# Kernel tuning notes

Hardware: AMD Instinct MI355X
Metric: run time of the kernel (lower is better)

## Reference

```python
import jax, jax.numpy as jnp
import numpy as np

B, IN, FS, S, H = 4096, 4096, 4096, 64, 512  # batch, input_size, first_size, shape_lstm, n_hidden
D = FS // S  # per-step feature for left/right (=64); up/down per-step feature = S (=64)


def _lstm_cell(x, h, c, Wih, Whh, bih, bhh):
    # standard torch LSTMCell gate order: i, f, g, o
    g = x @ Wih.T + bih + h @ Whh.T + bhh  # (B, 4H)
    i, f, gg, o = jnp.split(g, 4, axis=-1)
    c = jax.nn.sigmoid(f) * c + jax.nn.sigmoid(i) * jnp.tanh(gg)
    h = jax.nn.sigmoid(o) * jnp.tanh(c)
    return h, c


def setup_inputs() -> dict:
    key = jax.random.key(0)
    ks = jax.random.split(key, 20)
    def cell(k, d_in):
        k1, k2, k3, k4 = jax.random.split(k, 4)
        s = 1.0 / np.sqrt(H)
        return (jax.random.uniform(k1, (4 * H, d_in), jnp.float32, -s, s),
                jax.random.uniform(k2, (4 * H, H), jnp.float32, -s, s),
                jax.random.uniform(k3, (4 * H,), jnp.float32, -s, s),
                jax.random.uniform(k4, (4 * H,), jnp.float32, -s, s))
    Wih_l, Whh_l, bih_l, bhh_l = cell(ks[0], D)
    Wih_r, Whh_r, bih_r, bhh_r = cell(ks[1], D)
    Wih_d, Whh_d, bih_d, bhh_d = cell(ks[2], S)
    return {
        "x": jax.random.normal(ks[3], (B, IN), jnp.float32),
        "h0": jax.random.normal(ks[4], (4, B, H), jnp.float32),
        "c0": jax.random.normal(ks[5], (4, B, H), jnp.float32),
        "W1": jax.random.normal(ks[6], (FS, IN), jnp.float32) * (1.0 / np.sqrt(IN)),
        "b1": jnp.zeros((FS,), jnp.float32),
        "Wih_l": Wih_l, "Whh_l": Whh_l, "bih_l": bih_l, "bhh_l": bhh_l,
        "Wih_r": Wih_r, "Whh_r": Whh_r, "bih_r": bih_r, "bhh_r": bhh_r,
        "Wih_d": Wih_d, "Whh_d": Whh_d, "bih_d": bih_d, "bhh_d": bhh_d,
        "W3": jax.random.normal(ks[7], (10, 4 * H), jnp.float32) * (1.0 / np.sqrt(4 * H)),
        "b3": jnp.zeros((10,), jnp.float32),
    }


def reference(x, h0, c0, W1, b1, Wih_l, Whh_l, bih_l, bhh_l,
              Wih_r, Whh_r, bih_r, bhh_r, Wih_d, Whh_d, bih_d, bhh_d, W3, b3):
    feat = jax.nn.relu(x @ W1.T + b1)            # (B, FS); dropout=identity (eval)
    il = feat.reshape(B, S, D)
    x_left = jnp.transpose(il, (1, 0, 2))         # (S, B, D)
    x_right = x_left[::-1]
    x_up = jnp.transpose(il, (2, 0, 1))           # (D, B, S); loop uses first S steps
    x_down = x_up[::-1]

    def step(carry, xs):
        (hl, cl, hr, cr, hu, cu, hd, cd) = carry
        xl, xr, xu, xd = xs
        hl, cl = _lstm_cell(xl, hl, cl, Wih_l, Whh_l, bih_l, bhh_l)
        hr, cr = _lstm_cell(xr, hr, cr, Wih_r, Whh_r, bih_r, bhh_r)
        # original code uses the DOWN cell for both up and down directions
        hu, cu = _lstm_cell(xu, hu, cu, Wih_d, Whh_d, bih_d, bhh_d)
        hd, cd = _lstm_cell(xd, hd, cd, Wih_d, Whh_d, bih_d, bhh_d)
        return (hl, cl, hr, cr, hu, cu, hd, cd), None

    carry0 = (h0[0], c0[0], h0[1], c0[1], h0[2], c0[2], h0[3], c0[3])
    (hl, _, hr, _, hu, _, hd, _), _ = jax.lax.scan(
        step, carry0, (x_left[:S], x_right[:S], x_up[:S], x_down[:S]))
    out = jnp.concatenate([hl, hr, hu, hd], axis=1)  # (B, 4H)
    logits = out @ W3.T + b3
    return jax.nn.log_softmax(logits, axis=1)
```

## Files before the change

### kernel.cpp

```cpp
#include <hip/hip_runtime.h>
#include <cstddef>
#include <cstdint>

namespace {

constexpr int kB  = 4096;
constexpr int kIN = 4096;
constexpr int kFS = 4096;
constexpr int kS  = 64;
constexpr int kH  = 512;
constexpr int kNG = 2048;
constexpr int kKC = 576;

typedef __bf16 bf16_t;
typedef __bf16 bfrag  __attribute__((ext_vector_type(8)));
typedef __bf16 bf16v4 __attribute__((ext_vector_type(4)));
typedef float  f32x4  __attribute__((ext_vector_type(4)));

__device__ __forceinline__ void gload16(const void* g, void* l) {
  __builtin_amdgcn_global_load_lds(
      (const __attribute__((address_space(1))) void*)g,
      (__attribute__((address_space(3))) void*)l, 16, 0, 0);
}

__device__ __forceinline__ float sigf(float x) { return 1.0f / (1.0f + __expf(-x)); }
__device__ __forceinline__ float tanh_fast(float x) {
  float e = __expf(2.0f * x);
  return 1.0f - 2.0f / (e + 1.0f);
}

__device__ __forceinline__ f32x4 mfma16(bfrag a, bfrag b, f32x4 c) {
  return __builtin_amdgcn_mfma_f32_16x16x32_bf16(a, b, c, 0, 0, 0);
}


__global__ __launch_bounds__(256) void f2b4_kernel(const float* __restrict__ in,
                                                   bf16_t* __restrict__ out, int n4) {
  int i = blockIdx.x * 256 + threadIdx.x;
  if (i >= n4) return;
  float4 v = reinterpret_cast<const float4*>(in)[i];
  bf16v4 o = {(bf16_t)v.x, (bf16_t)v.y, (bf16_t)v.z, (bf16_t)v.w};
  *reinterpret_cast<bf16v4*>(out + (size_t)i * 4) = o;
}

__global__ __launch_bounds__(256) void pack_wcat2_kernel(
    const float* __restrict__ Wih_l, const float* __restrict__ Whh_l,
    const float* __restrict__ Wih_r, const float* __restrict__ Whh_r,
    const float* __restrict__ Wih_d, const float* __restrict__ Whh_d,
    bf16_t* __restrict__ wcat2) {
  const int total = 3 * 128 * 9 * 2 * 64 * 8;
  int idx = blockIdx.x * 256 + threadIdx.x;
  if (idx >= total) return;
  int e  = idx & 7;
  int l  = (idx >> 3) & 63;
  int kk = (idx >> 9) & 1;
  int r  = idx >> 10;
  int kt = r % 9;
  int matnb = r / 9;
  int mat = matnb >> 7;
  int nb  = matnb & 127;
  const int c = nb * 16 + (l & 15);
  const int g = (c >> 4) & 3;
  const int u = (c >> 6) * 16 + (c & 15);
  const int orow = g * kH + u;
  const int k = kt * 64 + kk * 32 + (l >> 4) * 8 + e;
  const float* Wih = (mat == 0) ? Wih_l : (mat == 1) ? Wih_r : Wih_d;
  const float* Whh = (mat == 0) ? Whh_l : (mat == 1) ? Whh_r : Whh_d;
  float v = (k < 64) ? Wih[(size_t)orow * 64 + k] : Whh[(size_t)orow * 512 + (k - 64)];
  wcat2[idx] = (bf16_t)v;
}

__global__ __launch_bounds__(256) void pack_bias_kernel(
    const float* __restrict__ bih_l, const float* __restrict__ bhh_l,
    const float* __restrict__ bih_r, const float* __restrict__ bhh_r,
    const float* __restrict__ bih_d, const float* __restrict__ bhh_d,
    float* __restrict__ biasc) {
  int idx = blockIdx.x * 256 + threadIdx.x;
  if (idx >= 3 * kNG) return;
  int mat = idx / kNG;
  int c = idx - mat * kNG;
  int g = (c >> 4) & 3;
  int u = (c >> 6) * 16 + (c & 15);
  int orow = g * kH + u;
  const float* bi = (mat == 0) ? bih_l : (mat == 1) ? bih_r : bih_d;
  const float* bh = (mat == 0) ? bhh_l : (mat == 1) ? bhh_r : bhh_d;
  biasc[idx] = bi[orow] + bh[orow];
}

__global__ __launch_bounds__(256) void pack_hc_kernel(const float* __restrict__ h0,
                                                      const float* __restrict__ c0,
                                                      bf16_t* __restrict__ hbuf0,
                                                      float* __restrict__ cbuf, int n) {
  int i = blockIdx.x * 256 + threadIdx.x;
  if (i >= n) return;
  hbuf0[i] = (bf16_t)h0[i];
  cbuf[i]  = c0[i];
}

__global__ __launch_bounds__(256) void transpose64_kernel(const bf16_t* __restrict__ feat,
                                                          bf16_t* __restrict__ featT) {
  __shared__ bf16_t tile[64][65];
  const int b = blockIdx.x;
  const bf16_t* src = feat + (size_t)b * kFS;
  bf16_t* dst = featT + (size_t)b * kFS;
  for (int i = threadIdx.x; i < 4096; i += 256) tile[i >> 6][i & 63] = src[i];
  __syncthreads();
  for (int i = threadIdx.x; i < 4096; i += 256) dst[i] = tile[i & 63][i >> 6];
}


__global__ __launch_bounds__(256, 4) void gemm_feat_kernel(
    const bf16_t* __restrict__ X, const bf16_t* __restrict__ W,
    const float* __restrict__ b1, bf16_t* __restrict__ feat) {
  __shared__ bf16_t As[128 * 32];
  __shared__ bf16_t Bs[128 * 32];
  const int t = threadIdx.x;
  const int bid = blockIdx.x;
  const int widx = (bid & 7) * 128 + (bid >> 3);
  const int bm = widx & 31, bn = widx >> 5;
  const int w = t >> 6, l = t & 63;
  const int wm = (w >> 1) * 64, wn = (w & 1) * 64;
  const int sr = t >> 2;
  const int skS = ((t & 3) ^ ((t >> 3) & 3)) * 8;
  const int lr = l & 15;
  const int lkS = ((l >> 4) ^ ((l >> 1) & 3)) * 8;
  const int lrow4 = (l >> 4) * 4;

  f32x4 acc[4][4];
#pragma unroll
  for (int i = 0; i < 4; ++i)
#pragma unroll
    for (int j = 0; j < 4; ++j) acc[i][j] = (f32x4){0.f, 0.f, 0.f, 0.f};

  const bf16_t* ga = X + (size_t)(bm * 128 + sr) * kIN + skS;
  const bf16_t* gb = W + (size_t)(bn * 128 + sr) * kIN + skS;
  bf16_t* lA = As + w * 512;
  bf16_t* lB = Bs + w * 512;

  for (int kt = 0; kt < kIN / 32; ++kt) {
    gload16(ga, lA);
    gload16(ga + (size_t)64 * kIN, lA + 2048);
    gload16(gb, lB);
    gload16(gb + (size_t)64 * kIN, lB + 2048);
    ga += 32; gb += 32;
    __syncthreads();
    bfrag a[4], b[4];
#pragma unroll
    for (int mi = 0; mi < 4; ++mi)
      a[mi] = *reinterpret_cast<const bfrag*>(&As[(wm + mi * 16 + lr) * 32 + lkS]);
#pragma unroll
    for (int ni = 0; ni < 4; ++ni)
      b[ni] = *reinterpret_cast<const bfrag*>(&Bs[(wn + ni * 16 + lr) * 32 + lkS]);
#pragma unroll
    for (int mi = 0; mi < 4; ++mi)
#pragma unroll
      for (int ni = 0; ni < 4; ++ni)
        acc[mi][ni] = __builtin_amdgcn_mfma_f32_16x16x32_bf16(a[mi], b[ni], acc[mi][ni], 0, 0, 0);
    __syncthreads();
  }

#pragma unroll
  for (int ni = 0; ni < 4; ++ni) {
    const int col = bn * 128 + wn + ni * 16 + lr;
    const float bb = b1[col];
#pragma unroll
    for (int mi = 0; mi < 4; ++mi) {
#pragma unroll
      for (int r = 0; r < 4; ++r) {
        const int row = bm * 128 + wm + mi * 16 + lrow4 + r;
        float v = acc[mi][ni][r] + bb;
        feat[(size_t)row * kFS + col] = (bf16_t)fmaxf(v, 0.0f);
      }
    }
  }
}


__global__ __launch_bounds__(512, 1) void lstm_step_kernel(
    const bf16_t* __restrict__ feat, const bf16_t* __restrict__ featT,
    const bf16_t* __restrict__ wcat2, const float* __restrict__ biasc,
    const bf16_t* __restrict__ hin, bf16_t* __restrict__ hout,
    float* __restrict__ cbuf, int s) {
  extern __shared__ __align__(16) char smem[];

  const int t = threadIdx.x;
  const int l = t & 63, w = t >> 6;
  const int wr = w >> 2, wc = w & 3;
  const int lr = l & 15, lq = l >> 4;
  const int sx = lr & 7;
  const int srow = l >> 3;
  const int sslot = (l & 7) ^ (srow & 7);

  const int bid = blockIdx.x;
  const int widx = (bid & 7) * 64 + (bid >> 3);
  const int cell = widx >> 7;
  const int rwk = widx & 127;
  const int bm = rwk >> 3, bn = rwk & 7;

  const bf16_t* xsrc = (cell < 2) ? feat : featT;
  const int off = ((cell & 1) ? (63 - s) : s) * 64;
  const int mat = (cell < 2) ? cell : 2;
  const bf16_t* hc = hin + (size_t)cell * kB * kH;

  auto stageA = [&](int kt, int buf) {
    bf16_t* base = (bf16_t*)(smem + buf * 32768);
#pragma unroll
    for (int j = 0; j < 4; ++j) {
      const int row0 = j * 64 + w * 8;
      bf16_t* dst = base + row0 * 64;
      const bf16_t* src = (kt == 0)
          ? xsrc + (size_t)(bm * 256 + row0 + srow) * kFS + off + sslot * 8
          : hc + (size_t)(bm * 256 + row0 + srow) * kH + (kt - 1) * 64 + sslot * 8;
      gload16(src, dst);
    }
  };

  const size_t wb0 = ((size_t)mat * 128 + bn * 16 + wc * 4) * 9;
  auto loadB = [&](int kt, bfrag (&d)[8]) {
#pragma unroll
    for (int nn = 0; nn < 4; ++nn)
#pragma unroll
      for (int kk = 0; kk < 2; ++kk)
        d[nn * 2 + kk] = *reinterpret_cast<const bfrag*>(
            wcat2 + (((wb0 + (size_t)nn * 9 + kt) * 2 + kk) << 9) + l * 8);
  };

  f32x4 acc[8][4];
#pragma unroll
  for (int i = 0; i < 8; ++i)
#pragma unroll
    for (int j = 0; j < 4; ++j) acc[i][j] = (f32x4){0.f, 0.f, 0.f, 0.f};

  bfrag bA[8], bB[8];

  stageA(0, 0);
  loadB(0, bA);
  asm volatile("s_waitcnt vmcnt(0)" ::: "memory");
  __builtin_amdgcn_sched_barrier(0);
  __builtin_amdgcn_s_barrier();

#pragma unroll
  for (int kt = 0; kt < 9; ++kt) {
    const int cur = kt & 1;
    const bf16_t* As_ = (const bf16_t*)(smem + cur * 32768);
    bfrag (&bCur)[8] = (kt & 1) ? bB : bA;
    bfrag (&bNxt)[8] = (kt & 1) ? bA : bB;

    if (kt < 8) stageA(kt + 1, cur ^ 1);

    bfrag a[8];
#pragma unroll
    for (int mi = 0; mi < 4; ++mi)
#pragma unroll
      for (int kk = 0; kk < 2; ++kk)
        a[mi * 2 + kk] = *reinterpret_cast<const bfrag*>(
            As_ + (wr * 128 + mi * 16 + lr) * 64 + (((kk * 4 + lq) ^ sx) * 8));
    __builtin_amdgcn_s_setprio(1);
#pragma unroll
    for (int kk = 0; kk < 2; ++kk)
#pragma unroll
      for (int mi = 0; mi < 4; ++mi)
#pragma unroll
        for (int nn = 0; nn < 4; ++nn)
          acc[mi][nn] = mfma16(a[mi * 2 + kk], bCur[nn * 2 + kk], acc[mi][nn]);
    __builtin_amdgcn_s_setprio(0);

    if (kt < 8) loadB(kt + 1, bNxt);

#pragma unroll
    for (int mi = 0; mi < 4; ++mi)
#pragma unroll
      for (int kk = 0; kk < 2; ++kk)
        a[mi * 2 + kk] = *reinterpret_cast<const bfrag*>(
            As_ + (wr * 128 + 64 + mi * 16 + lr) * 64 + (((kk * 4 + lq) ^ sx) * 8));
    __builtin_amdgcn_s_setprio(1);
#pragma unroll
    for (int kk = 0; kk < 2; ++kk)
#pragma unroll
      for (int mi = 0; mi < 4; ++mi)
#pragma unroll
        for (int nn = 0; nn < 4; ++nn)
          acc[4 + mi][nn] = mfma16(a[mi * 2 + kk], bCur[nn * 2 + kk], acc[4 + mi][nn]);
    __builtin_amdgcn_s_setprio(0);
    __builtin_amdgcn_sched_barrier(0);

    if (kt < 8) {
      asm volatile("s_waitcnt vmcnt(8)" ::: "memory");
      __builtin_amdgcn_sched_barrier(0);
      __builtin_amdgcn_s_barrier();
    }
  }

  const float* biasn = biasc + mat * kNG + bn * 256 + wc * 64;
  const float bb0 = biasn[0 * 16 + lr];
  const float bb1 = biasn[1 * 16 + lr];
  const float bb2 = biasn[2 * 16 + lr];
  const float bb3 = biasn[3 * 16 + lr];
  const int u = (bn * 4 + wc) * 16 + lr;
  const int row0 = bm * 256 + wr * 128 + lq * 4;
#pragma unroll
  for (int mi = 0; mi < 8; ++mi) {
#pragma unroll
    for (int j = 0; j < 4; ++j) {
      const float iv = sigf(acc[mi][0][j] + bb0);
      const float fv = sigf(acc[mi][1][j] + bb1);
      const float gv = tanh_fast(acc[mi][2][j] + bb2);
      const float ov = sigf(acc[mi][3][j] + bb3);
      const int row = row0 + mi * 16 + j;
      const size_t cidx = ((size_t)cell * kB + row) * kH + u;
      const float cn = fv * cbuf[cidx] + iv * gv;
      cbuf[cidx] = cn;
      hout[cidx] = (bf16_t)(ov * tanh_fast(cn));
    }
  }
}


__global__ __launch_bounds__(256) void head_kernel(const bf16_t* __restrict__ hfin,
                                                   const float* __restrict__ W3,
                                                   const float* __restrict__ b3,
                                                   float* __restrict__ out) {
  const int b = blockIdx.x, t = threadIdx.x;
  const int l = t & 63, w = t >> 6;
  float acc[10];
#pragma unroll
  for (int j = 0; j < 10; ++j) acc[j] = 0.f;
  for (int k = t; k < 2048; k += 256) {
    const int cell = k >> 9, u = k & 511;
    const float hv = (float)hfin[((size_t)cell * kB + b) * kH + u];
#pragma unroll
    for (int j = 0; j < 10; ++j) acc[j] += hv * W3[j * 2048 + k];
  }
#pragma unroll
  for (int j = 0; j < 10; ++j)
#pragma unroll
    for (int o = 32; o > 0; o >>= 1) acc[j] += __shfl_down(acc[j], o, 64);
  __shared__ float wred[4][10];
  if (l == 0)
#pragma unroll
    for (int j = 0; j < 10; ++j) wred[w][j] = acc[j];
  __syncthreads();
  if (t == 0) {
    float logits[10];
#pragma unroll
    for (int j = 0; j < 10; ++j)
      logits[j] = wred[0][j] + wred[1][j] + wred[2][j] + wred[3][j] + b3[j];
    float mx = logits[0];
#pragma unroll
    for (int j = 1; j < 10; ++j) mx = fmaxf(mx, logits[j]);
    float se = 0.f;
#pragma unroll
    for (int j = 0; j < 10; ++j) se += expf(logits[j] - mx);
    const float lse = mx + logf(se);
#pragma unroll
    for (int j = 0; j < 10; ++j) out[(size_t)b * 10 + j] = logits[j] - lse;
  }
}

}

extern "C" void kernel_launch(void* const* d_in, const int* in_sizes, int n_in,
                              void* d_out, int out_size, void* d_ws, size_t ws_size,
                              hipStream_t stream) {
  const float* x     = (const float*)d_in[0];
  const float* h0    = (const float*)d_in[1];
  const float* c0    = (const float*)d_in[2];
  const float* W1    = (const float*)d_in[3];
  const float* b1    = (const float*)d_in[4];
  const float* Wih_l = (const float*)d_in[5];
  const float* Whh_l = (const float*)d_in[6];
  const float* bih_l = (const float*)d_in[7];
  const float* bhh_l = (const float*)d_in[8];
  const float* Wih_r = (const float*)d_in[9];
  const float* Whh_r = (const float*)d_in[10];
  const float* bih_r = (const float*)d_in[11];
  const float* bhh_r = (const float*)d_in[12];
  const float* Wih_d = (const float*)d_in[13];
  const float* Whh_d = (const float*)d_in[14];
  const float* bih_d = (const float*)d_in[15];
  const float* bhh_d = (const float*)d_in[16];
  const float* W3    = (const float*)d_in[17];
  const float* b3    = (const float*)d_in[18];
  float* out = (float*)d_out;

  char* p = (char*)d_ws;
  auto take = [&](size_t bytes) {
    char* r = p;
    p += (bytes + 255) & ~(size_t)255;
    return r;
  };
  bf16_t* xb    = (bf16_t*)take((size_t)kB * kIN * 2);
  bf16_t* w1b   = (bf16_t*)take((size_t)kFS * kIN * 2);
  bf16_t* feat  = (bf16_t*)take((size_t)kB * kFS * 2);
  bf16_t* wcat2 = (bf16_t*)take((size_t)3 * 128 * 9 * 2 * 64 * 8 * 2);
  float*  biasc = (float*)take((size_t)3 * kNG * 4);
  float*  cbuf  = (float*)take((size_t)4 * kB * kH * 4);
  bf16_t* featT = xb;
  bf16_t* hbuf  = w1b;
  const size_t HSZ = (size_t)4 * kB * kH;

  (void)hipFuncSetAttribute(reinterpret_cast<const void*>(&lstm_step_kernel),
                            hipFuncAttributeMaxDynamicSharedMemorySize, 65536);

  f2b4_kernel<<<(kB * kIN / 4) / 256, 256, 0, stream>>>(x, xb, kB * kIN / 4);
  f2b4_kernel<<<(kFS * kIN / 4) / 256, 256, 0, stream>>>(W1, w1b, kFS * kIN / 4);
  gemm_feat_kernel<<<dim3(1024), 256, 0, stream>>>(xb, w1b, b1, feat);
  transpose64_kernel<<<kB, 256, 0, stream>>>(feat, featT);
  {
    const int total = 3 * 128 * 9 * 2 * 64 * 8;
    pack_wcat2_kernel<<<(total + 255) / 256, 256, 0, stream>>>(
        Wih_l, Whh_l, Wih_r, Whh_r, Wih_d, Whh_d, wcat2);
  }
  pack_bias_kernel<<<(3 * kNG + 255) / 256, 256, 0, stream>>>(
      bih_l, bhh_l, bih_r, bhh_r, bih_d, bhh_d, biasc);
  pack_hc_kernel<<<(int)(HSZ / 256), 256, 0, stream>>>(h0, c0, hbuf, cbuf, (int)HSZ);

  for (int s = 0; s < 64; ++s) {
    lstm_step_kernel<<<dim3(512), 512, 65536, stream>>>(
        feat, featT, wcat2, biasc,
        hbuf + (size_t)(s & 1) * HSZ, hbuf + (size_t)((s + 1) & 1) * HSZ, cbuf, s);
  }
  head_kernel<<<kB, 256, 0, stream>>>(hbuf, W3, b3, out);
}
```

Measured before the change: 3.834 ms.

## Fuse all 64 LSTM steps into one persistent kernel with h kept in LDS

Replaces the 64 per-step LSTM launches with a single persistent kernel of 256 blocks. Each block owns 64 batch rows of one direction across all gate columns, so the recurrent hidden state stays in shared memory and no global h round-trip or inter-block sync is needed. h0/c0 packing is folded into the kernel, and the cell state is kept in a block-private layout in global memory. In exchange, only 256 blocks run, and all weights are streamed from global/L2 every step by each block, which may lower parallelism and raise weight traffic.

```diff
diff --git a/kernel.cpp b/kernel.cpp
--- a/kernel.cpp
+++ b/kernel.cpp
@@ -11,6 +11,7 @@
 constexpr int kH  = 512;
 constexpr int kNG = 2048;
 constexpr int kKC = 576;
+constexpr int kRowB = 1152;
 
 typedef __bf16 bf16_t;
 typedef __bf16 bfrag  __attribute__((ext_vector_type(8)));
@@ -28,9 +29,12 @@
   float e = __expf(2.0f * x);
   return 1.0f - 2.0f / (e + 1.0f);
 }
-
 __device__ __forceinline__ f32x4 mfma16(bfrag a, bfrag b, f32x4 c) {
   return __builtin_amdgcn_mfma_f32_16x16x32_bf16(a, b, c, 0, 0, 0);
+}
+__device__ __forceinline__ unsigned short bf16bits(float v) {
+  __bf16 b = (__bf16)v;
+  return __builtin_bit_cast(unsigned short, b);
 }
 
 
@@ -87,16 +91,6 @@
   biasc[idx] = bi[orow] + bh[orow];
 }
 
-__global__ __launch_bounds__(256) void pack_hc_kernel(const float* __restrict__ h0,
-                                                      const float* __restrict__ c0,
-                                                      bf16_t* __restrict__ hbuf0,
-                                                      float* __restrict__ cbuf, int n) {
-  int i = blockIdx.x * 256 + threadIdx.x;
-  if (i >= n) return;
-  hbuf0[i] = (bf16_t)h0[i];
-  cbuf[i]  = c0[i];
-}
-
 __global__ __launch_bounds__(256) void transpose64_kernel(const bf16_t* __restrict__ feat,
                                                           bf16_t* __restrict__ featT) {
   __shared__ bf16_t tile[64][65];
@@ -176,142 +170,166 @@
 }
 
 
-__global__ __launch_bounds__(512, 1) void lstm_step_kernel(
+__global__ __launch_bounds__(512, 1) void lstm_all_kernel(
     const bf16_t* __restrict__ feat, const bf16_t* __restrict__ featT,
     const bf16_t* __restrict__ wcat2, const float* __restrict__ biasc,
-    const bf16_t* __restrict__ hin, bf16_t* __restrict__ hout,
-    float* __restrict__ cbuf, int s) {
+    const float* __restrict__ h0, const float* __restrict__ c0,
+    float* __restrict__ cbuf, bf16_t* __restrict__ hfin) {
   extern __shared__ __align__(16) char smem[];
 
   const int t = threadIdx.x;
   const int l = t & 63, w = t >> 6;
-  const int wr = w >> 2, wc = w & 3;
   const int lr = l & 15, lq = l >> 4;
   const int sx = lr & 7;
-  const int srow = l >> 3;
-  const int sslot = (l & 7) ^ (srow & 7);
+  const int e0 = lq ^ sx;
+  const int e1 = (4 + lq) ^ sx;
 
   const int bid = blockIdx.x;
-  const int widx = (bid & 7) * 64 + (bid >> 3);
-  const int cell = widx >> 7;
-  const int rwk = widx & 127;
-  const int bm = rwk >> 3, bn = rwk & 7;
-
+  const int cell = (bid & 7) >> 1;
+  const int rb = ((bid & 7) & 1) * 32 + (bid >> 3);
+  const int row0 = rb * 64;
+  const int mat = (cell < 2) ? cell : 2;
   const bf16_t* xsrc = (cell < 2) ? feat : featT;
-  const int off = ((cell & 1) ? (63 - s) : s) * 64;
-  const int mat = (cell < 2) ? cell : 2;
-  const bf16_t* hc = hin + (size_t)cell * kB * kH;
-
-  auto stageA = [&](int kt, int buf) {
-    bf16_t* base = (bf16_t*)(smem + buf * 32768);
-#pragma unroll
-    for (int j = 0; j < 4; ++j) {
-      const int row0 = j * 64 + w * 8;
-      bf16_t* dst = base + row0 * 64;
-      const bf16_t* src = (kt == 0)
-          ? xsrc + (size_t)(bm * 256 + row0 + srow) * kFS + off + sslot * 8
-          : hc + (size_t)(bm * 256 + row0 + srow) * kH + (kt - 1) * 64 + sslot * 8;
-      gload16(src, dst);
-    }
-  };
-
-  const size_t wb0 = ((size_t)mat * 128 + bn * 16 + wc * 4) * 9;
-  auto loadB = [&](int kt, bfrag (&d)[8]) {
+
+  const char* aBase[4][2];
+#pragma unroll
+  for (int mi = 0; mi < 4; ++mi) {
+    const int rowb = (mi * 16 + lr) * kRowB;
+    aBase[mi][0] = smem + rowb + e0 * 16;
+    aBase[mi][1] = smem + rowb + e1 * 16;
+  }
+
+  const size_t nbBase = (size_t)mat * 128 + w * 4;
+  auto loadB = [&](int ch, int kt, bfrag (&d)[8]) {
 #pragma unroll
     for (int nn = 0; nn < 4; ++nn)
 #pragma unroll
       for (int kk = 0; kk < 2; ++kk)
         d[nn * 2 + kk] = *reinterpret_cast<const bfrag*>(
-            wcat2 + (((wb0 + (size_t)nn * 9 + kt) * 2 + kk) << 9) + l * 8);
+            wcat2 + ((((nbBase + ch * 32 + nn) * 9 + kt) * 2 + kk) << 9) + l * 8);
   };
 
-  f32x4 acc[8][4];
-#pragma unroll
-  for (int i = 0; i < 8; ++i)
+  {
+    const int xr = t >> 3, xs_ = t & 7;
+    bfrag xv = *reinterpret_cast<const bfrag*>(
+        xsrc + (size_t)(row0 + xr) * kFS + ((cell & 1) ? 63 : 0) * 64 + xs_ * 8);
+    *reinterpret_cast<bfrag*>(smem + xr * kRowB + ((xs_ ^ (xr & 7)) * 16)) = xv;
+    const int u0 = (t & 7) * 64;
+    const float* hp = h0 + ((size_t)cell * kB + row0 + xr) * kH + u0;
+#pragma unroll
+    for (int i = 0; i < 8; ++i) {
+      bfrag hv;
+#pragma unroll
+      for (int e = 0; e < 8; ++e) hv[e] = (bf16_t)hp[i * 8 + e];
+      const int sl = (8 + (u0 >> 3) + i) ^ (xr & 7);
+      *reinterpret_cast<bfrag*>(smem + xr * kRowB + sl * 16) = hv;
+    }
+  }
+  __syncthreads();
+
+  f32x4 acc[4][4];
+#pragma unroll
+  for (int i = 0; i < 4; ++i)
 #pragma unroll
     for (int j = 0; j < 4; ++j) acc[i][j] = (f32x4){0.f, 0.f, 0.f, 0.f};
 
-  bfrag bA[8], bB[8];
-
-  stageA(0, 0);
-  loadB(0, bA);
-  asm volatile("s_waitcnt vmcnt(0)" ::: "memory");
-  __builtin_amdgcn_sched_barrier(0);
-  __builtin_amdgcn_s_barrier();
-
-#pragma unroll
-  for (int kt = 0; kt < 9; ++kt) {
-    const int cur = kt & 1;
-    const bf16_t* As_ = (const bf16_t*)(smem + cur * 32768);
-    bfrag (&bCur)[8] = (kt & 1) ? bB : bA;
-    bfrag (&bNxt)[8] = (kt & 1) ? bA : bB;
-
-    if (kt < 8) stageA(kt + 1, cur ^ 1);
-
-    bfrag a[8];
-#pragma unroll
-    for (int mi = 0; mi < 4; ++mi)
-#pragma unroll
-      for (int kk = 0; kk < 2; ++kk)
-        a[mi * 2 + kk] = *reinterpret_cast<const bfrag*>(
-            As_ + (wr * 128 + mi * 16 + lr) * 64 + (((kk * 4 + lq) ^ sx) * 8));
-    __builtin_amdgcn_s_setprio(1);
-#pragma unroll
-    for (int kk = 0; kk < 2; ++kk)
-#pragma unroll
-      for (int mi = 0; mi < 4; ++mi)
-#pragma unroll
-        for (int nn = 0; nn < 4; ++nn)
-          acc[mi][nn] = mfma16(a[mi * 2 + kk], bCur[nn * 2 + kk], acc[mi][nn]);
-    __builtin_amdgcn_s_setprio(0);
-
-    if (kt < 8) loadB(kt + 1, bNxt);
-
-#pragma unroll
-    for (int mi = 0; mi < 4; ++mi)
-#pragma unroll
-      for (int kk = 0; kk < 2; ++kk)
-        a[mi * 2 + kk] = *reinterpret_cast<const bfrag*>(
-            As_ + (wr * 128 + 64 + mi * 16 + lr) * 64 + (((kk * 4 + lq) ^ sx) * 8));
-    __builtin_amdgcn_s_setprio(1);
-#pragma unroll
-    for (int kk = 0; kk < 2; ++kk)
-#pragma unroll
-      for (int mi = 0; mi < 4; ++mi)
-#pragma unroll
-        for (int nn = 0; nn < 4; ++nn)
-          acc[4 + mi][nn] = mfma16(a[mi * 2 + kk], bCur[nn * 2 + kk], acc[4 + mi][nn]);
-    __builtin_amdgcn_s_setprio(0);
-    __builtin_amdgcn_sched_barrier(0);
-
-    if (kt < 8) {
-      asm volatile("s_waitcnt vmcnt(8)" ::: "memory");
-      __builtin_amdgcn_sched_barrier(0);
-      __builtin_amdgcn_s_barrier();
+  bfrag bE[8], bO[8];
+  unsigned hpk[4][8];
+  loadB(0, 0, bE);
+
+#pragma unroll 1
+  for (int s = 0; s < 64; ++s) {
+#pragma unroll
+    for (int ch = 0; ch < 4; ++ch) {
+#pragma unroll
+      for (int kt = 0; kt < 9; ++kt) {
+        const int i = ch * 9 + kt;
+        bfrag (&bc)[8] = (i & 1) ? bO : bE;
+        bfrag (&bn_)[8] = (i & 1) ? bE : bO;
+        if (i < 35) loadB((i + 1) / 9, (i + 1) % 9, bn_);
+        else        loadB(0, 0, bn_);
+        bfrag a[8];
+#pragma unroll
+        for (int mi = 0; mi < 4; ++mi) {
+          a[mi * 2 + 0] = *reinterpret_cast<const bfrag*>(aBase[mi][0] + kt * 128);
+          a[mi * 2 + 1] = *reinterpret_cast<const bfrag*>(aBase[mi][1] + kt * 128);
+        }
+#pragma unroll
+        for (int kk = 0; kk < 2; ++kk)
+#pragma unroll
+          for (int mi = 0; mi < 4; ++mi)
+#pragma unroll
+            for (int nn = 0; nn < 4; ++nn)
+              acc[mi][nn] = mfma16(a[mi * 2 + kk], bc[nn * 2 + kk], acc[mi][nn]);
+      }
+      {
+        const float* bbp = biasc + mat * kNG + ch * 512 + w * 64;
+        const float bb0 = bbp[lr], bb1 = bbp[16 + lr], bb2 = bbp[32 + lr], bb3 = bbp[48 + lr];
+        const int u = (ch * 8 + w) * 16 + lr;
+        float* cp = cbuf + ((((size_t)bid * 4 + ch) * 8 + w) * 64 + l) * 16;
+#pragma unroll
+        for (int mi = 0; mi < 4; ++mi) {
+          float cv[4];
+          if (s == 0) {
+            const float* c0p = c0 + ((size_t)cell * kB + row0 + mi * 16 + lq * 4) * kH + u;
+#pragma unroll
+            for (int j = 0; j < 4; ++j) cv[j] = c0p[(size_t)j * kH];
+          } else {
+            float4 c4 = reinterpret_cast<const float4*>(cp)[mi];
+            cv[0] = c4.x; cv[1] = c4.y; cv[2] = c4.z; cv[3] = c4.w;
+          }
+          float hv[4];
+#pragma unroll
+          for (int j = 0; j < 4; ++j) {
+            const float iv = sigf(acc[mi][0][j] + bb0);
+            const float fv = sigf(acc[mi][1][j] + bb1);
+            const float gv = tanh_fast(acc[mi][2][j] + bb2);
+            const float ov = sigf(acc[mi][3][j] + bb3);
+            const float cn = fv * cv[j] + iv * gv;
+            cv[j] = cn;
+            hv[j] = ov * tanh_fast(cn);
+          }
+          reinterpret_cast<float4*>(cp)[mi] = make_float4(cv[0], cv[1], cv[2], cv[3]);
+          if (s < 63) {
+            hpk[ch][mi * 2 + 0] = (unsigned)bf16bits(hv[0]) | ((unsigned)bf16bits(hv[1]) << 16);
+            hpk[ch][mi * 2 + 1] = (unsigned)bf16bits(hv[2]) | ((unsigned)bf16bits(hv[3]) << 16);
+          } else {
+#pragma unroll
+            for (int j = 0; j < 4; ++j)
+              hfin[((size_t)cell * kB + row0 + mi * 16 + lq * 4 + j) * kH + u] = (bf16_t)hv[j];
+          }
+#pragma unroll
+          for (int nn = 0; nn < 4; ++nn) acc[mi][nn] = (f32x4){0.f, 0.f, 0.f, 0.f};
+        }
+      }
     }
-  }
-
-  const float* biasn = biasc + mat * kNG + bn * 256 + wc * 64;
-  const float bb0 = biasn[0 * 16 + lr];
-  const float bb1 = biasn[1 * 16 + lr];
-  const float bb2 = biasn[2 * 16 + lr];
-  const float bb3 = biasn[3 * 16 + lr];
-  const int u = (bn * 4 + wc) * 16 + lr;
-  const int row0 = bm * 256 + wr * 128 + lq * 4;
-#pragma unroll
-  for (int mi = 0; mi < 8; ++mi) {
-#pragma unroll
-    for (int j = 0; j < 4; ++j) {
-      const float iv = sigf(acc[mi][0][j] + bb0);
-      const float fv = sigf(acc[mi][1][j] + bb1);
-      const float gv = tanh_fast(acc[mi][2][j] + bb2);
-      const float ov = sigf(acc[mi][3][j] + bb3);
-      const int row = row0 + mi * 16 + j;
-      const size_t cidx = ((size_t)cell * kB + row) * kH + u;
-      const float cn = fv * cbuf[cidx] + iv * gv;
-      cbuf[cidx] = cn;
-      hout[cidx] = (bf16_t)(ov * tanh_fast(cn));
+    __syncthreads();
+    if (s < 63) {
+#pragma unroll
+      for (int ch = 0; ch < 4; ++ch) {
+        const int u = (ch * 8 + w) * 16 + lr;
+        const int sl = 8 + (u >> 3);
+        const int eb = (u & 7) * 2;
+#pragma unroll
+        for (int mi = 0; mi < 4; ++mi)
+#pragma unroll
+          for (int p = 0; p < 2; ++p) {
+            const unsigned v = hpk[ch][mi * 2 + p];
+            const int r0 = mi * 16 + lq * 4 + p * 2;
+            *reinterpret_cast<uint16_t*>(smem + r0 * kRowB + ((sl ^ (r0 & 7)) * 16) + eb) =
+                (uint16_t)v;
+            const int r1 = r0 + 1;
+            *reinterpret_cast<uint16_t*>(smem + r1 * kRowB + ((sl ^ (r1 & 7)) * 16) + eb) =
+                (uint16_t)(v >> 16);
+          }
+      }
+      const int xr = t >> 3, xs_ = t & 7;
+      const int offn = ((cell & 1) ? (63 - (s + 1)) : (s + 1)) * 64;
+      bfrag xv = *reinterpret_cast<const bfrag*>(
+          xsrc + (size_t)(row0 + xr) * kFS + offn + xs_ * 8);
+      *reinterpret_cast<bfrag*>(smem + xr * kRowB + ((xs_ ^ (xr & 7)) * 16)) = xv;
     }
+    __syncthreads();
   }
 }
 
@@ -396,11 +414,10 @@
   float*  biasc = (float*)take((size_t)3 * kNG * 4);
   float*  cbuf  = (float*)take((size_t)4 * kB * kH * 4);
   bf16_t* featT = xb;
-  bf16_t* hbuf  = w1b;
-  const size_t HSZ = (size_t)4 * kB * kH;
-
-  (void)hipFuncSetAttribute(reinterpret_cast<const void*>(&lstm_step_kernel),
-                            hipFuncAttributeMaxDynamicSharedMemorySize, 65536);
+  bf16_t* hfin  = w1b;
+
+  (void)hipFuncSetAttribute(reinterpret_cast<const void*>(&lstm_all_kernel),
+                            hipFuncAttributeMaxDynamicSharedMemorySize, 64 * kRowB);
 
   f2b4_kernel<<<(kB * kIN / 4) / 256, 256, 0, stream>>>(x, xb, kB * kIN / 4);
   f2b4_kernel<<<(kFS * kIN / 4) / 256, 256, 0, stream>>>(W1, w1b, kFS * kIN / 4);
@@ -413,12 +430,9 @@
   }
   pack_bias_kernel<<<(3 * kNG + 255) / 256, 256, 0, stream>>>(
       bih_l, bhh_l, bih_r, bhh_r, bih_d, bhh_d, biasc);
-  pack_hc_kernel<<<(int)(HSZ / 256), 256, 0, stream>>>(h0, c0, hbuf, cbuf, (int)HSZ);
-
-  for (int s = 0; s < 64; ++s) {
-    lstm_step_kernel<<<dim3(512), 512, 65536, stream>>>(
-        feat, featT, wcat2, biasc,
-        hbuf + (size_t)(s & 1) * HSZ, hbuf + (size_t)((s + 1) & 1) * HSZ, cbuf, s);
-  }
-  head_kernel<<<kB, 256, 0, stream>>>(hbuf, W3, b3, out);
-}
+
+  lstm_all_kernel<<<dim3(256), 512, 64 * kRowB, stream>>>(
+      feat, featT, wcat2, biasc, h0, c0, cbuf, hfin);
+
+  head_kernel<<<kB, 256, 0, stream>>>(hfin, W3, b3, out);
+}
```

Result: slower. 13.80 ms (+259.8%).

## Shrink LSTM step tiles to 128x128 with 256-thread blocks for occupancy

Applied to the files above, without the earlier changes.

Each LSTM step block now covers a 128-row by 128-gate-column tile using 4 waves, replacing the 256x256 tile and 8 waves, so the grid grows from 512 to 2048 blocks and targets 3 blocks per CU with half the LDS. The next B-fragment prefetch is also issued before the MFMA work rather than midway through it. The aim is more resident waves to hide global-load latency and better balance across CUs. The trade-off is less reuse of A and B per block, so more redundant global and L2 traffic for weights and activations.

```diff
diff --git a/kernel.cpp b/kernel.cpp
--- a/kernel.cpp
+++ b/kernel.cpp
@@ -28,7 +28,6 @@
   float e = __expf(2.0f * x);
   return 1.0f - 2.0f / (e + 1.0f);
 }
-
 __device__ __forceinline__ f32x4 mfma16(bfrag a, bfrag b, f32x4 c) {
   return __builtin_amdgcn_mfma_f32_16x16x32_bf16(a, b, c, 0, 0, 0);
 }
@@ -176,7 +175,7 @@
 }
 
 
-__global__ __launch_bounds__(512, 1) void lstm_step_kernel(
+__global__ __launch_bounds__(256, 3) void lstm_step_kernel(
     const bf16_t* __restrict__ feat, const bf16_t* __restrict__ featT,
     const bf16_t* __restrict__ wcat2, const float* __restrict__ biasc,
     const bf16_t* __restrict__ hin, bf16_t* __restrict__ hout,
@@ -185,17 +184,17 @@
 
   const int t = threadIdx.x;
   const int l = t & 63, w = t >> 6;
-  const int wr = w >> 2, wc = w & 3;
+  const int wr = w >> 1, wcn = w & 1;
   const int lr = l & 15, lq = l >> 4;
   const int sx = lr & 7;
   const int srow = l >> 3;
-  const int sslot = (l & 7) ^ (srow & 7);
+  const int sslot = (l & 7) ^ srow;
 
   const int bid = blockIdx.x;
-  const int widx = (bid & 7) * 64 + (bid >> 3);
-  const int cell = widx >> 7;
-  const int rwk = widx & 127;
-  const int bm = rwk >> 3, bn = rwk & 7;
+  const int widx = (bid & 7) * 256 + (bid >> 3);
+  const int cell = widx >> 9;
+  const int rwk = widx & 511;
+  const int bm = rwk >> 4, bn = rwk & 15;
 
   const bf16_t* xsrc = (cell < 2) ? feat : featT;
   const int off = ((cell & 1) ? (63 - s) : s) * 64;
@@ -203,38 +202,38 @@
   const bf16_t* hc = hin + (size_t)cell * kB * kH;
 
   auto stageA = [&](int kt, int buf) {
-    bf16_t* base = (bf16_t*)(smem + buf * 32768);
+    bf16_t* base = (bf16_t*)(smem + buf * 16384);
 #pragma unroll
     for (int j = 0; j < 4; ++j) {
-      const int row0 = j * 64 + w * 8;
+      const int row0 = j * 32 + w * 8;
       bf16_t* dst = base + row0 * 64;
       const bf16_t* src = (kt == 0)
-          ? xsrc + (size_t)(bm * 256 + row0 + srow) * kFS + off + sslot * 8
-          : hc + (size_t)(bm * 256 + row0 + srow) * kH + (kt - 1) * 64 + sslot * 8;
+          ? xsrc + (size_t)(bm * 128 + row0 + srow) * kFS + off + sslot * 8
+          : hc + (size_t)(bm * 128 + row0 + srow) * kH + (kt - 1) * 64 + sslot * 8;
       gload16(src, dst);
     }
   };
 
-  const size_t wb0 = ((size_t)mat * 128 + bn * 16 + wc * 4) * 9;
+  const size_t nbB = (size_t)mat * 128 + bn * 8 + wcn * 4;
   auto loadB = [&](int kt, bfrag (&d)[8]) {
 #pragma unroll
     for (int nn = 0; nn < 4; ++nn)
 #pragma unroll
       for (int kk = 0; kk < 2; ++kk)
         d[nn * 2 + kk] = *reinterpret_cast<const bfrag*>(
-            wcat2 + (((wb0 + (size_t)nn * 9 + kt) * 2 + kk) << 9) + l * 8);
+            wcat2 + ((((nbB + nn) * 9 + kt) * 2 + kk) << 9) + l * 8);
   };
 
-  f32x4 acc[8][4];
-#pragma unroll
-  for (int i = 0; i < 8; ++i)
+  f32x4 acc[4][4];
+#pragma unroll
+  for (int i = 0; i < 4; ++i)
 #pragma unroll
     for (int j = 0; j < 4; ++j) acc[i][j] = (f32x4){0.f, 0.f, 0.f, 0.f};
 
-  bfrag bA[8], bB[8];
+  bfrag bE[8], bO[8];
 
   stageA(0, 0);
-  loadB(0, bA);
+  loadB(0, bE);
   asm volatile("s_waitcnt vmcnt(0)" ::: "memory");
   __builtin_amdgcn_sched_barrier(0);
   __builtin_amdgcn_s_barrier();
@@ -242,48 +241,30 @@
 #pragma unroll
   for (int kt = 0; kt < 9; ++kt) {
     const int cur = kt & 1;
-    const bf16_t* As_ = (const bf16_t*)(smem + cur * 32768);
-    bfrag (&bCur)[8] = (kt & 1) ? bB : bA;
-    bfrag (&bNxt)[8] = (kt & 1) ? bA : bB;
-
-    if (kt < 8) stageA(kt + 1, cur ^ 1);
-
-    bfrag a[8];
-#pragma unroll
-    for (int mi = 0; mi < 4; ++mi)
-#pragma unroll
-      for (int kk = 0; kk < 2; ++kk)
-        a[mi * 2 + kk] = *reinterpret_cast<const bfrag*>(
-            As_ + (wr * 128 + mi * 16 + lr) * 64 + (((kk * 4 + lq) ^ sx) * 8));
-    __builtin_amdgcn_s_setprio(1);
-#pragma unroll
-    for (int kk = 0; kk < 2; ++kk)
+    if (kt < 8) {
+      stageA(kt + 1, cur ^ 1);
+      __builtin_amdgcn_sched_barrier(0);
+      if (kt & 1) loadB(kt + 1, bE); else loadB(kt + 1, bO);
+      __builtin_amdgcn_sched_barrier(0);
+    }
+    const bf16_t* As_ = (const bf16_t*)(smem + cur * 16384);
+#pragma unroll
+    for (int kk = 0; kk < 2; ++kk) {
+      bfrag a[4];
 #pragma unroll
       for (int mi = 0; mi < 4; ++mi)
+        a[mi] = *reinterpret_cast<const bfrag*>(
+            As_ + (wr * 64 + mi * 16 + lr) * 64 + (((kk * 4 + lq) ^ sx) * 8));
+      __builtin_amdgcn_s_setprio(1);
+#pragma unroll
+      for (int mi = 0; mi < 4; ++mi)
 #pragma unroll
         for (int nn = 0; nn < 4; ++nn)
-          acc[mi][nn] = mfma16(a[mi * 2 + kk], bCur[nn * 2 + kk], acc[mi][nn]);
-    __builtin_amdgcn_s_setprio(0);
-
-    if (kt < 8) loadB(kt + 1, bNxt);
-
-#pragma unroll
-    for (int mi = 0; mi < 4; ++mi)
-#pragma unroll
-      for (int kk = 0; kk < 2; ++kk)
-        a[mi * 2 + kk] = *reinterpret_cast<const bfrag*>(
-            As_ + (wr * 128 + 64 + mi * 16 + lr) * 64 + (((kk * 4 + lq) ^ sx) * 8));
-    __builtin_amdgcn_s_setprio(1);
-#pragma unroll
-    for (int kk = 0; kk < 2; ++kk)
-#pragma unroll
-      for (int mi = 0; mi < 4; ++mi)
-#pragma unroll
-        for (int nn = 0; nn < 4; ++nn)
-          acc[4 + mi][nn] = mfma16(a[mi * 2 + kk], bCur[nn * 2 + kk], acc[4 + mi][nn]);
-    __builtin_amdgcn_s_setprio(0);
+          acc[mi][nn] = (kt & 1) ? mfma16(a[mi], bO[nn * 2 + kk], acc[mi][nn])
+                                 : mfma16(a[mi], bE[nn * 2 + kk], acc[mi][nn]);
+      __builtin_amdgcn_s_setprio(0);
+    }
     __builtin_amdgcn_sched_barrier(0);
-
     if (kt < 8) {
       asm volatile("s_waitcnt vmcnt(8)" ::: "memory");
       __builtin_amdgcn_sched_barrier(0);
@@ -291,22 +272,23 @@
     }
   }
 
-  const float* biasn = biasc + mat * kNG + bn * 256 + wc * 64;
-  const float bb0 = biasn[0 * 16 + lr];
-  const float bb1 = biasn[1 * 16 + lr];
-  const float bb2 = biasn[2 * 16 + lr];
-  const float bb3 = biasn[3 * 16 + lr];
-  const int u = (bn * 4 + wc) * 16 + lr;
-  const int row0 = bm * 256 + wr * 128 + lq * 4;
-#pragma unroll
-  for (int mi = 0; mi < 8; ++mi) {
+  const int nb0 = bn * 8 + wcn * 4;
+  const float* bbp = biasc + mat * kNG + nb0 * 16;
+  const float bb0 = bbp[lr];
+  const float bb1 = bbp[16 + lr];
+  const float bb2 = bbp[32 + lr];
+  const float bb3 = bbp[48 + lr];
+  const int u = (bn * 2 + wcn) * 16 + lr;
+  const int row0g = bm * 128 + wr * 64 + lq * 4;
+#pragma unroll
+  for (int mi = 0; mi < 4; ++mi) {
 #pragma unroll
     for (int j = 0; j < 4; ++j) {
       const float iv = sigf(acc[mi][0][j] + bb0);
       const float fv = sigf(acc[mi][1][j] + bb1);
       const float gv = tanh_fast(acc[mi][2][j] + bb2);
       const float ov = sigf(acc[mi][3][j] + bb3);
-      const int row = row0 + mi * 16 + j;
+      const int row = row0g + mi * 16 + j;
       const size_t cidx = ((size_t)cell * kB + row) * kH + u;
       const float cn = fv * cbuf[cidx] + iv * gv;
       cbuf[cidx] = cn;
@@ -400,7 +382,7 @@
   const size_t HSZ = (size_t)4 * kB * kH;
 
   (void)hipFuncSetAttribute(reinterpret_cast<const void*>(&lstm_step_kernel),
-                            hipFuncAttributeMaxDynamicSharedMemorySize, 65536);
+                            hipFuncAttributeMaxDynamicSharedMemorySize, 32768);
 
   f2b4_kernel<<<(kB * kIN / 4) / 256, 256, 0, stream>>>(x, xb, kB * kIN / 4);
   f2b4_kernel<<<(kFS * kIN / 4) / 256, 256, 0, stream>>>(W1, w1b, kFS * kIN / 4);
@@ -416,7 +398,7 @@
   pack_hc_kernel<<<(int)(HSZ / 256), 256, 0, stream>>>(h0, c0, hbuf, cbuf, (int)HSZ);
 
   for (int s = 0; s < 64; ++s) {
-    lstm_step_kernel<<<dim3(512), 512, 65536, stream>>>(
+    lstm_step_kernel<<<dim3(2048), 256, 32768, stream>>>(
         feat, featT, wcat2, biasc,
         hbuf + (size_t)(s & 1) * HSZ, hbuf + (size_t)((s + 1) & 1) * HSZ, cbuf, s);
   }
```

Result: slower. 4.129 ms (+7.7%).

## Rewrite feature GEMM with 256x256 tiles, fragment-packed W1, double-buffered LDS

Applied to the files above, without the earlier changes.

Replaces the 128x128 feature GEMM with a 256x256-tile, 512-thread kernel. W1 is pre-packed into MFMA fragment order so B operands load straight from global into registers and are prefetched one tile ahead, while A tiles are double-buffered in swizzled LDS. The goal is more reuse per block, fewer barriers and overlap of loads with MFMAs. The tradeoff is higher register pressure with one block per CU, only 256 blocks, and a scattered, uncoalesced read of W1 in the pack kernel.

```diff
diff --git a/kernel.cpp b/kernel.cpp
--- a/kernel.cpp
+++ b/kernel.cpp
@@ -41,6 +41,20 @@
   float4 v = reinterpret_cast<const float4*>(in)[i];
   bf16v4 o = {(bf16_t)v.x, (bf16_t)v.y, (bf16_t)v.z, (bf16_t)v.w};
   *reinterpret_cast<bf16v4*>(out + (size_t)i * 4) = o;
+}
+
+__global__ __launch_bounds__(256) void pack_w1frag_kernel(const float* __restrict__ W1,
+                                                          bf16_t* __restrict__ w1f) {
+  int idx = blockIdx.x * 256 + threadIdx.x;
+  int e  = idx & 7;
+  int l  = (idx >> 3) & 63;
+  int kk = (idx >> 9) & 1;
+  int r  = idx >> 10;
+  int kt = r & 63;
+  int nb = r >> 6;
+  const int col = nb * 16 + (l & 15);
+  const int k = kt * 64 + kk * 32 + (l >> 4) * 8 + e;
+  w1f[idx] = (bf16_t)W1[(size_t)col * kIN + k];
 }
 
 __global__ __launch_bounds__(256) void pack_wcat2_kernel(
@@ -109,67 +123,123 @@
 }
 
 
-__global__ __launch_bounds__(256, 4) void gemm_feat_kernel(
-    const bf16_t* __restrict__ X, const bf16_t* __restrict__ W,
+__global__ __launch_bounds__(512, 1) void gemm_feat256_kernel(
+    const bf16_t* __restrict__ X, const bf16_t* __restrict__ w1f,
     const float* __restrict__ b1, bf16_t* __restrict__ feat) {
-  __shared__ bf16_t As[128 * 32];
-  __shared__ bf16_t Bs[128 * 32];
+  extern __shared__ __align__(16) char smem[];
+
   const int t = threadIdx.x;
+  const int l = t & 63, w = t >> 6;
+  const int wr = w >> 2, wc = w & 3;
+  const int lr = l & 15, lq = l >> 4;
+  const int sx = lr & 7;
+  const int srow = l >> 3;
+  const int sslot = (l & 7) ^ (srow & 7);
+
   const int bid = blockIdx.x;
-  const int widx = (bid & 7) * 128 + (bid >> 3);
-  const int bm = widx & 31, bn = widx >> 5;
-  const int w = t >> 6, l = t & 63;
-  const int wm = (w >> 1) * 64, wn = (w & 1) * 64;
-  const int sr = t >> 2;
-  const int skS = ((t & 3) ^ ((t >> 3) & 3)) * 8;
-  const int lr = l & 15;
-  const int lkS = ((l >> 4) ^ ((l >> 1) & 3)) * 8;
-  const int lrow4 = (l >> 4) * 4;
-
-  f32x4 acc[4][4];
-#pragma unroll
-  for (int i = 0; i < 4; ++i)
+  const int widx = (bid & 7) * 32 + (bid >> 3);
+  const int bn = widx >> 4, bm = widx & 15;
+
+  auto stageA = [&](int kt, int buf) {
+    bf16_t* base = (bf16_t*)(smem + buf * 32768);
+#pragma unroll
+    for (int j = 0; j < 4; ++j) {
+      const int row0 = j * 64 + w * 8;
+      bf16_t* dst = base + row0 * 64;
+      const bf16_t* src =
+          X + (size_t)(bm * 256 + row0 + srow) * kIN + kt * 64 + sslot * 8;
+      gload16(src, dst);
+    }
+  };
+
+  auto loadB = [&](int kt, bfrag (&d)[8]) {
+#pragma unroll
+    for (int nn = 0; nn < 4; ++nn) {
+      const int nb = bn * 16 + wc * 4 + nn;
+#pragma unroll
+      for (int kk = 0; kk < 2; ++kk)
+        d[nn * 2 + kk] = *reinterpret_cast<const bfrag*>(
+            w1f + ((((size_t)nb * 64 + kt) * 2 + kk) << 9) + l * 8);
+    }
+  };
+
+  f32x4 acc[8][4];
+#pragma unroll
+  for (int i = 0; i < 8; ++i)
 #pragma unroll
     for (int j = 0; j < 4; ++j) acc[i][j] = (f32x4){0.f, 0.f, 0.f, 0.f};
 
-  const bf16_t* ga = X + (size_t)(bm * 128 + sr) * kIN + skS;
-  const bf16_t* gb = W + (size_t)(bn * 128 + sr) * kIN + skS;
-  bf16_t* lA = As + w * 512;
-  bf16_t* lB = Bs + w * 512;
-
-  for (int kt = 0; kt < kIN / 32; ++kt) {
-    gload16(ga, lA);
-    gload16(ga + (size_t)64 * kIN, lA + 2048);
-    gload16(gb, lB);
-    gload16(gb + (size_t)64 * kIN, lB + 2048);
-    ga += 32; gb += 32;
-    __syncthreads();
-    bfrag a[4], b[4];
+  bfrag bA[8], bB[8];
+
+  stageA(0, 0);
+  loadB(0, bA);
+  asm volatile("s_waitcnt vmcnt(0)" ::: "memory");
+  __builtin_amdgcn_sched_barrier(0);
+  __builtin_amdgcn_s_barrier();
+
+  auto tileBody = [&](int kt, int cur, bfrag (&bCur)[8], bfrag (&bNxt)[8], bool last) {
+    const bf16_t* As_ = (const bf16_t*)(smem + cur * 32768);
+    if (!last) stageA(kt + 1, cur ^ 1);
+    bfrag a[8];
 #pragma unroll
     for (int mi = 0; mi < 4; ++mi)
-      a[mi] = *reinterpret_cast<const bfrag*>(&As[(wm + mi * 16 + lr) * 32 + lkS]);
-#pragma unroll
-    for (int ni = 0; ni < 4; ++ni)
-      b[ni] = *reinterpret_cast<const bfrag*>(&Bs[(wn + ni * 16 + lr) * 32 + lkS]);
+#pragma unroll
+      for (int kk = 0; kk < 2; ++kk)
+        a[mi * 2 + kk] = *reinterpret_cast<const bfrag*>(
+            As_ + (wr * 128 + mi * 16 + lr) * 64 + (((kk * 4 + lq) ^ sx) * 8));
+    __builtin_amdgcn_s_setprio(1);
+#pragma unroll
+    for (int kk = 0; kk < 2; ++kk)
+#pragma unroll
+      for (int mi = 0; mi < 4; ++mi)
+#pragma unroll
+        for (int nn = 0; nn < 4; ++nn)
+          acc[mi][nn] = mfma16(a[mi * 2 + kk], bCur[nn * 2 + kk], acc[mi][nn]);
+    __builtin_amdgcn_s_setprio(0);
+    if (!last) loadB(kt + 1, bNxt);
 #pragma unroll
     for (int mi = 0; mi < 4; ++mi)
 #pragma unroll
-      for (int ni = 0; ni < 4; ++ni)
-        acc[mi][ni] = __builtin_amdgcn_mfma_f32_16x16x32_bf16(a[mi], b[ni], acc[mi][ni], 0, 0, 0);
-    __syncthreads();
-  }
-
-#pragma unroll
-  for (int ni = 0; ni < 4; ++ni) {
-    const int col = bn * 128 + wn + ni * 16 + lr;
-    const float bb = b1[col];
-#pragma unroll
-    for (int mi = 0; mi < 4; ++mi) {
-#pragma unroll
-      for (int r = 0; r < 4; ++r) {
-        const int row = bm * 128 + wm + mi * 16 + lrow4 + r;
-        float v = acc[mi][ni][r] + bb;
-        feat[(size_t)row * kFS + col] = (bf16_t)fmaxf(v, 0.0f);
+      for (int kk = 0; kk < 2; ++kk)
+        a[mi * 2 + kk] = *reinterpret_cast<const bfrag*>(
+            As_ + (wr * 128 + 64 + mi * 16 + lr) * 64 + (((kk * 4 + lq) ^ sx) * 8));
+    __builtin_amdgcn_s_setprio(1);
+#pragma unroll
+    for (int kk = 0; kk < 2; ++kk)
+#pragma unroll
+      for (int mi = 0; mi < 4; ++mi)
+#pragma unroll
+        for (int nn = 0; nn < 4; ++nn)
+          acc[4 + mi][nn] = mfma16(a[mi * 2 + kk], bCur[nn * 2 + kk], acc[4 + mi][nn]);
+    __builtin_amdgcn_s_setprio(0);
+    __builtin_amdgcn_sched_barrier(0);
+    if (!last) {
+      asm volatile("s_waitcnt vmcnt(8)" ::: "memory");
+      __builtin_amdgcn_sched_barrier(0);
+      __builtin_amdgcn_s_barrier();
+    }
+  };
+
+#pragma unroll 1
+  for (int kt2 = 0; kt2 < 32; ++kt2) {
+    tileBody(2 * kt2, 0, bA, bB, false);
+    tileBody(2 * kt2 + 1, 1, bB, bA, kt2 == 31);
+  }
+
+  const int row0 = bm * 256 + wr * 128 + lq * 4;
+  float bb[4];
+#pragma unroll
+  for (int nn = 0; nn < 4; ++nn)
+    bb[nn] = b1[bn * 256 + (wc * 4 + nn) * 16 + lr];
+#pragma unroll
+  for (int mi = 0; mi < 8; ++mi) {
+#pragma unroll
+    for (int nn = 0; nn < 4; ++nn) {
+      const int col = bn * 256 + (wc * 4 + nn) * 16 + lr;
+#pragma unroll
+      for (int j = 0; j < 4; ++j) {
+        const int row = row0 + mi * 16 + j;
+        feat[(size_t)row * kFS + col] = (bf16_t)fmaxf(acc[mi][nn][j] + bb[nn], 0.0f);
       }
     }
   }
@@ -390,21 +460,23 @@
     return r;
   };
   bf16_t* xb    = (bf16_t*)take((size_t)kB * kIN * 2);
-  bf16_t* w1b   = (bf16_t*)take((size_t)kFS * kIN * 2);
+  bf16_t* w1f   = (bf16_t*)take((size_t)kFS * kIN * 2);
   bf16_t* feat  = (bf16_t*)take((size_t)kB * kFS * 2);
   bf16_t* wcat2 = (bf16_t*)take((size_t)3 * 128 * 9 * 2 * 64 * 8 * 2);
   float*  biasc = (float*)take((size_t)3 * kNG * 4);
   float*  cbuf  = (float*)take((size_t)4 * kB * kH * 4);
   bf16_t* featT = xb;
-  bf16_t* hbuf  = w1b;
+  bf16_t* hbuf  = w1f;
   const size_t HSZ = (size_t)4 * kB * kH;
 
   (void)hipFuncSetAttribute(reinterpret_cast<const void*>(&lstm_step_kernel),
                             hipFuncAttributeMaxDynamicSharedMemorySize, 65536);
+  (void)hipFuncSetAttribute(reinterpret_cast<const void*>(&gemm_feat256_kernel),
+                            hipFuncAttributeMaxDynamicSharedMemorySize, 65536);
 
   f2b4_kernel<<<(kB * kIN / 4) / 256, 256, 0, stream>>>(x, xb, kB * kIN / 4);
-  f2b4_kernel<<<(kFS * kIN / 4) / 256, 256, 0, stream>>>(W1, w1b, kFS * kIN / 4);
-  gemm_feat_kernel<<<dim3(1024), 256, 0, stream>>>(xb, w1b, b1, feat);
+  pack_w1frag_kernel<<<(kFS * kIN) / 256, 256, 0, stream>>>(W1, w1f);
+  gemm_feat256_kernel<<<dim3(256), 512, 65536, stream>>>(xb, w1f, b1, feat);
   transpose64_kernel<<<kB, 256, 0, stream>>>(feat, featT);
   {
     const int total = 3 * 128 * 9 * 2 * 64 * 8;
```

New measurement: 3.862 ms. About the same (+0.7%).
